# Kernel tuning notes

Measured on AMD Instinct MI355X. Metric: run time of the kernel, lower is better.

## Reference

```python
import jax, jax.numpy as jnp
import numpy as np

N, E, D_IN, H, C = 100000, 1600000, 256, 128, 10


def setup_inputs() -> dict:
    key = jax.random.key(0)
    ks = jax.random.split(key, 12)
    x = jax.random.normal(ks[0], (N, D_IN), dtype=jnp.float32)
    edge_index = jax.random.randint(ks[1], (2, E), 0, N, dtype=jnp.int64)
    reranker_scores = jax.random.normal(ks[2], (N,), dtype=jnp.float32)
    s_in = 1.0 / np.sqrt(D_IN)
    s_h = 1.0 / np.sqrt(H)
    # SAGEConv: lin_l applies to aggregated neighbors (with bias), lin_r to root (no bias)
    W_l = jax.random.uniform(ks[3], (H, D_IN), jnp.float32, -s_in, s_in)
    b_l = jax.random.uniform(ks[4], (H,), jnp.float32, -s_in, s_in)
    W_r = jax.random.uniform(ks[5], (H, D_IN), jnp.float32, -s_in, s_in)
    W_res = jax.random.uniform(ks[6], (H, D_IN), jnp.float32, -s_in, s_in)
    b_res = jax.random.uniform(ks[7], (H,), jnp.float32, -s_in, s_in)
    W_score = jax.random.uniform(ks[8], (1, H), jnp.float32, -s_h, s_h)
    b_score = jax.random.uniform(ks[9], (1,), jnp.float32, -s_h, s_h)
    W_crit = jax.random.uniform(ks[10], (C, H), jnp.float32, -s_h, s_h)
    b_crit = jax.random.uniform(ks[11], (C,), jnp.float32, -s_h, s_h)
    alpha = jnp.float32(0.65)
    return {"x": x, "edge_index": edge_index, "reranker_scores": reranker_scores,
            "W_l": W_l, "b_l": b_l, "W_r": W_r, "W_res": W_res, "b_res": b_res,
            "W_score": W_score, "b_score": b_score, "W_crit": W_crit, "b_crit": b_crit,
            "alpha": alpha}


def reference(x, edge_index, reranker_scores, W_l, b_l, W_r, W_res, b_res,
              W_score, b_score, W_crit, b_crit, alpha):
    src, dst = edge_index[0], edge_index[1]
    n = x.shape[0]
    ones = jnp.ones(src.shape[0], dtype=x.dtype)
    deg = jax.ops.segment_sum(ones, dst, num_segments=n)          # [N]
    nbr_sum = jax.ops.segment_sum(x[src], dst, num_segments=n)    # [N, D_IN]
    agg = nbr_sum / jnp.maximum(deg, 1.0)[:, None]                # mean aggregation
    # SAGEConv: lin_l(agg) + lin_r(x); relu; dropout (eval -> identity); residual
    h = jax.nn.relu(agg @ W_l.T + b_l + x @ W_r.T)                # [N, H]
    h = h + (x @ W_res.T + b_res)                                 # residual projection
    gnn_scores = (h @ W_score.T + b_score)[:, 0]                  # [N]
    a = jax.nn.sigmoid(alpha)
    final_scores = a * reranker_scores + (1.0 - a) * gnn_scores
    criterion_logits = h @ W_crit.T + b_crit                      # [N, C]
    return final_scores, criterion_logits
```

## Files before the change

kernel.cpp:

```cpp
#include <hip/hip_runtime.h>
#include <math.h>

#define DIN 256
#define HDIM 128
#define NCRIT 10
#define BSH 9
#define EPB 4096

typedef __bf16 bf16;
typedef bf16 bf16x8 __attribute__((ext_vector_type(8)));
typedef float f32x4 __attribute__((ext_vector_type(4)));
typedef float f32x2 __attribute__((ext_vector_type(2)));

static inline size_t alignup(size_t x, size_t a) { return (x + a - 1) & ~(a - 1); }

__device__ inline float bflo(unsigned v) { return __uint_as_float(v << 16); }
__device__ inline float bfhi(unsigned v) { return __uint_as_float(v & 0xffff0000u); }

__device__ inline bf16x8 cvt8(float4 v0, float4 v1) {
    bf16x8 w;
    w[0] = (bf16)v0.x; w[1] = (bf16)v0.y; w[2] = (bf16)v0.z; w[3] = (bf16)v0.w;
    w[4] = (bf16)v1.x; w[5] = (bf16)v1.y; w[6] = (bf16)v1.z; w[7] = (bf16)v1.w;
    return w;
}

__device__ inline void gl_lds16(const void* g, void* l) {
    __builtin_amdgcn_global_load_lds(
        (const __attribute__((address_space(1))) unsigned*)g,
        (__attribute__((address_space(3))) unsigned*)l, 16, 0, 0);
}

__global__ __launch_bounds__(256) void k_bucket2(
    const int* __restrict__ src, const int* __restrict__ dst, int E,
    int* __restrict__ bcnt, int2* __restrict__ bpool, int capb, int nB,
    const float* __restrict__ Wl, const float* __restrict__ Wr,
    const float* __restrict__ Wres,
    const float* __restrict__ wscore, const float* __restrict__ wcrit,
    bf16* __restrict__ WcatT)
{
    int t = threadIdx.x;
    int b = blockIdx.x;
    if (b < 64) {
        int base = (b * 256 + t) * 4;
        int r = base >> 8;
        int c0 = base & 255;
        const float* W = (r < 128) ? Wl : Wr;
        float4 v = *(const float4*)&W[(size_t)(r & 127) * 256 + c0];
        bf16 o[4] = {(bf16)v.x, (bf16)v.y, (bf16)v.z, (bf16)v.w};
        char* d = (char*)WcatT + ((((size_t)(c0 >> 3) * 272 + r) << 4) + ((c0 & 7) << 1));
        *(uint2*)d = *(const uint2*)o;
        return;
    } else if (b < 80) {
        int q = b - 64;
        int k = t;
        float s = 0.f;
        if (q < 11) {
            const float* wepi = (q == 0) ? wscore : &wcrit[(size_t)(q - 1) * HDIM];
            for (int c = 0; c < HDIM; ++c)
                s += wepi[c] * Wres[(size_t)c * 256 + k];
        }
        char* d = (char*)WcatT + ((((size_t)(k >> 3) * 272 + 256 + q) << 4) + ((k & 7) << 1));
        *(bf16*)d = (bf16)s;
        return;
    }

    __shared__ int lcnt[256], lbase[256], lcur[256], gbase[256];
    __shared__ int2 stage[EPB];

    int blk = b - 80;
    int base = blk * EPB;
    int m = min(EPB, E - base);
    if (m <= 0) return;

    lcnt[t] = 0;
    __syncthreads();
    for (int i = t; i < m; i += 256)
        atomicAdd(&lcnt[dst[base + i] >> BSH], 1);
    __syncthreads();
    int c0 = lcnt[t];
    for (int d = 1; d < 256; d <<= 1) {
        int a0 = lcnt[t];
        int b0 = (t >= d) ? lcnt[t - d] : 0;
        __syncthreads();
        lcnt[t] = a0 + b0;
        __syncthreads();
    }
    int e0 = lcnt[t] - c0;
    lbase[t] = e0;
    lcur[t] = e0;
    if (t < nB && c0 > 0) gbase[t] = atomicAdd(&bcnt[t * 16], c0);
    __syncthreads();
    for (int i = t; i < m; i += 256) {
        int s2 = src[base + i], d = dst[base + i];
        int bk = d >> BSH;
        int pos = atomicAdd(&lcur[bk], 1);
        stage[pos] = make_int2(s2, d);
    }
    __syncthreads();
    int wv = t >> 6, lane = t & 63;
    for (int bk = wv; bk < nB; bk += 4) {
        int lb = lbase[bk];
        int cb = lcnt[bk] - lb;
        if (cb == 0) continue;
        int gb = gbase[bk];
        int2* dstp = bpool + (size_t)bk * capb + gb;
        for (int j = lane; j < cb && gb + j < capb; j += 64)
            dstp[j] = stage[lb + j];
    }
}

__global__ __launch_bounds__(256) void k_fin(const int* __restrict__ bcnt,
                                             const int2* __restrict__ bpool, int capb,
                                             int n, int* __restrict__ off,
                                             int* __restrict__ cnt, int* __restrict__ sidx) {
    __shared__ int lcnt[512], lcur[512];
    int b = blockIdx.x, t = threadIdx.x;
    int m = min(bcnt[b * 16], capb);
    const int2* ep = bpool + (size_t)b * capb;

    lcnt[t] = 0; lcnt[t + 256] = 0;
    __syncthreads();
    for (int i = t; i < m; i += 256) {
        int2 e = ep[i];
        atomicAdd(&lcnt[e.y & 511], 1);
    }
    __syncthreads();
    int c0 = lcnt[t], c1 = lcnt[t + 256];
    for (int d = 1; d < 512; d <<= 1) {
        int a0 = lcnt[t], a1 = lcnt[t + 256];
        int b0 = (t >= d) ? lcnt[t - d] : 0;
        int b1 = ((t + 256) >= d) ? lcnt[t + 256 - d] : 0;
        __syncthreads();
        lcnt[t] = a0 + b0; lcnt[t + 256] = a1 + b1;
        __syncthreads();
    }
    int e0 = lcnt[t] - c0, e1 = lcnt[t + 256] - c1;
    int nbase = b << BSH;
    int sbase = b * capb;
    lcur[t] = e0; lcur[t + 256] = e1;
    int n0 = nbase + t, n1 = nbase + t + 256;
    if (n0 < n) { off[n0] = sbase + e0; cnt[n0] = c0; }
    if (n1 < n) { off[n1] = sbase + e1; cnt[n1] = c1; }
    __syncthreads();
    for (int i = t; i < m; i += 256) {
        int2 e = ep[i];
        int pos = atomicAdd(&lcur[e.y & 511], 1);
        sidx[sbase + pos] = e.x;
    }
}

__global__ __launch_bounds__(512) void k_gemm(
    const float* __restrict__ x, const bf16* __restrict__ WcatT, int n,
    unsigned char* __restrict__ yq, bf16* __restrict__ z, float* __restrict__ w)
{
    __shared__ __align__(16) char smem[147456];
    int t = threadIdx.x;
    int wv = t >> 6, lane = t & 63;
    int l15 = lane & 15, kq = lane >> 4;

    {
        int cbase0 = wv * 64;
        #pragma unroll
        for (int i = 0; i < 17; i++) {
            int cbase = i * 512 + cbase0;
            gl_lds16((const char*)WcatT + (((size_t)cbase + lane) << 4),
                     smem + ((size_t)cbase << 4));
        }
    }
    __syncthreads();

    char* scr = smem + 139264 + wv * 1024;
    int rrow = lane >> 2, rc4 = (lane & 3) * 4;

    int nTiles = (n + 127) >> 7;
    for (int tile = blockIdx.x; tile < nTiles; tile += gridDim.x) {
        int rowb = tile * 128 + wv * 16;
        int myrow = rowb + l15;
        const float* ap = x + (size_t)(myrow < n ? myrow : (n - 1)) * 256 + kq * 8;

        float4 xa[8], xb[8];
        #pragma unroll
        for (int s = 0; s < 8; s++) {
            xa[s] = *(const float4*)(ap + s * 32);
            xb[s] = *(const float4*)(ap + s * 32 + 4);
        }

        f32x4 acc[17];
        #pragma unroll
        for (int C = 0; C < 17; C++) acc[C] = (f32x4){0.f, 0.f, 0.f, 0.f};

        #pragma unroll
        for (int s = 0; s < 8; s++) {
            bf16x8 afr = cvt8(xa[s], xb[s]);
            int sbase = ((s * 4 + kq) * 272 + l15) << 4;
            #pragma unroll
            for (int C = 0; C < 17; C++) {
                bf16x8 b = *(const bf16x8*)(smem + sbase + C * 256);
                acc[C] = __builtin_amdgcn_mfma_f32_16x16x32_bf16(afr, b, acc[C], 0, 0, 0);
            }
        }

        int gr = rowb + rrow;
        bool ok = gr < n;
        #pragma unroll
        for (int C = 0; C < 17; C++) {
            #pragma unroll
            for (int j = 0; j < 4; j++)
                *(float*)(scr + ((((kq << 2) + j) * 16 + l15) << 2)) = acc[C][j];
            f32x4 vv = *(const f32x4*)(scr + ((rrow * 16 + rc4) << 2));
            if (C < 8) {
                unsigned pk = (unsigned)__builtin_amdgcn_cvt_pk_fp8_f32(vv[0], vv[1], 0, false);
                pk = (unsigned)__builtin_amdgcn_cvt_pk_fp8_f32(vv[2], vv[3], pk, true);
                if (ok) *(unsigned*)(yq + (size_t)gr * 128 + C * 16 + rc4) = pk;
            } else if (C < 16) {
                bf16 o[4] = {(bf16)vv[0], (bf16)vv[1], (bf16)vv[2], (bf16)vv[3]};
                if (ok) *(uint2*)((char*)z + (size_t)gr * 256 + (C - 8) * 32 + rc4 * 2) =
                            *(const uint2*)o;
            } else {
                if (ok) *(f32x4*)(w + (size_t)gr * 16 + rc4) = vv;
            }
        }
    }
}

__global__ __launch_bounds__(256) void k_gather(
    const unsigned char* __restrict__ yq, const bf16* __restrict__ z,
    const float* __restrict__ w,
    const int* __restrict__ off, const int* __restrict__ cnt, const int* __restrict__ sidx,
    const float* __restrict__ bl, const float* __restrict__ bres,
    const float* __restrict__ wscore, const float* __restrict__ bscore,
    const float* __restrict__ wcrit, const float* __restrict__ bcrit,
    const float* __restrict__ rrs, const float* __restrict__ palpha,
    int n, float* __restrict__ outF, float* __restrict__ outL)
{
    __shared__ bf16 wsb[11 * 128];
    int t = threadIdx.x;
    for (int i = t; i < 11 * 128; i += 256) {
        int q = i >> 7, c = i & 127;
        wsb[i] = (bf16)((q == 0) ? wscore[c] : wcrit[(size_t)(q - 1) * HDIM + c]);
    }
    __syncthreads();

    int node = blockIdx.x * 4 + (t >> 6);
    if (node >= n) return;
    int lane = t & 63, r2 = lane >> 5, c32 = lane & 31;

    uint2 zr = *(const uint2*)&z[(size_t)node * HDIM + c32 * 4];
    float wpre = (lane < 16) ? w[(size_t)node * 16 + lane] : 0.f;
    float4 blv = *(const float4*)&bl[c32 * 4];
    float4 brv = *(const float4*)&bres[c32 * 4];

    const unsigned char* ybase = yq + c32 * 4;
    int beg = off[node], len = cnt[node];
    const int* sp = sidx + beg;

    f32x2 a01 = {0.f, 0.f}, a23 = {0.f, 0.f};
    int e = 0;
    for (; e + 8 <= len; e += 8) {
        int i0 = sp[e + r2];
        int i1 = sp[e + 2 + r2];
        int i2 = sp[e + 4 + r2];
        int i3 = sp[e + 6 + r2];
        int v0 = *(const int*)(ybase + ((size_t)(unsigned)i0 << 7));
        int v1 = *(const int*)(ybase + ((size_t)(unsigned)i1 << 7));
        int v2 = *(const int*)(ybase + ((size_t)(unsigned)i2 << 7));
        int v3 = *(const int*)(ybase + ((size_t)(unsigned)i3 << 7));
        a01 += __builtin_amdgcn_cvt_pk_f32_fp8(v0, false)
             + __builtin_amdgcn_cvt_pk_f32_fp8(v1, false)
             + __builtin_amdgcn_cvt_pk_f32_fp8(v2, false)
             + __builtin_amdgcn_cvt_pk_f32_fp8(v3, false);
        a23 += __builtin_amdgcn_cvt_pk_f32_fp8(v0, true)
             + __builtin_amdgcn_cvt_pk_f32_fp8(v1, true)
             + __builtin_amdgcn_cvt_pk_f32_fp8(v2, true)
             + __builtin_amdgcn_cvt_pk_f32_fp8(v3, true);
    }
    for (; e < len; e += 2) {
        int slot = e + r2;
        int ii = sp[slot < len ? slot : len - 1];
        int v = *(const int*)(ybase + ((size_t)(unsigned)ii << 7));
        if (slot < len) {
            a01 += __builtin_amdgcn_cvt_pk_f32_fp8(v, false);
            a23 += __builtin_amdgcn_cvt_pk_f32_fp8(v, true);
        }
    }
    float a0 = a01[0], a1 = a01[1], a2 = a23[0], a3 = a23[1];
    a0 += __shfl_xor(a0, 32, 64);
    a1 += __shfl_xor(a1, 32, 64);
    a2 += __shfl_xor(a2, 32, 64);
    a3 += __shfl_xor(a3, 32, 64);
    float inv = 1.f / fmaxf((float)len, 1.f);

    float h0 = fmaxf(a0 * inv + blv.x + bflo(zr.x), 0.f) + brv.x;
    float h1 = fmaxf(a1 * inv + blv.y + bfhi(zr.x), 0.f) + brv.y;
    float h2 = fmaxf(a2 * inv + blv.z + bflo(zr.y), 0.f) + brv.z;
    float h3 = fmaxf(a3 * inv + blv.w + bfhi(zr.y), 0.f) + brv.w;

    float p[6], wq[6];
    #pragma unroll
    for (int qq = 0; qq < 6; qq++) {
        int q = r2 * 6 + qq;
        float s = 0.f;
        if (q < 11) {
            uint2 ww = *(const uint2*)&wsb[q * 128 + c32 * 4];
            s = h0 * bflo(ww.x) + h1 * bfhi(ww.x) + h2 * bflo(ww.y) + h3 * bfhi(ww.y);
        }
        #pragma unroll
        for (int d = 1; d < 32; d <<= 1)
            s += __shfl_xor(s, d, 64);
        p[qq] = s;
        wq[qq] = __shfl(wpre, (q < 11) ? q : 0, 64);
    }
    if ((lane & 31) == 0) {
        if (r2 == 0) {
            float al = palpha[0];
            float aa = 1.f / (1.f + expf(-al));
            outF[node] = aa * rrs[node] + (1.f - aa) * (p[0] + wq[0] + bscore[0]);
            #pragma unroll
            for (int qq = 1; qq < 6; qq++)
                outL[(size_t)node * NCRIT + qq - 1] = p[qq] + wq[qq] + bcrit[qq - 1];
        } else {
            #pragma unroll
            for (int qq = 0; qq < 5; qq++)
                outL[(size_t)node * NCRIT + 5 + qq] = p[qq] + wq[qq] + bcrit[5 + qq];
        }
    }
}

extern "C" void kernel_launch(void* const* d_in, const int* in_sizes, int n_in,
                              void* d_out, int out_size, void* d_ws, size_t ws_size,
                              hipStream_t stream) {
    const float* x      = (const float*)d_in[0];
    const int*   ei     = (const int*)d_in[1];
    const float* rrs    = (const float*)d_in[2];
    const float* Wl     = (const float*)d_in[3];
    const float* bl     = (const float*)d_in[4];
    const float* Wr     = (const float*)d_in[5];
    const float* Wres   = (const float*)d_in[6];
    const float* bres   = (const float*)d_in[7];
    const float* wscore = (const float*)d_in[8];
    const float* bscore = (const float*)d_in[9];
    const float* wcrit  = (const float*)d_in[10];
    const float* bcrit  = (const float*)d_in[11];
    const float* alpha  = (const float*)d_in[12];

    int N = in_sizes[0] / DIN;
    int E = in_sizes[1] / 2;
    const int* srcv = ei;
    const int* dstv = ei + E;

    int nB = (N + 511) >> BSH;
    int capb = (E / (nB > 0 ? nB : 1)) * 2 + 256;

    char* p = (char*)d_ws;
    int* bcnt  = (int*)p; p += alignup((size_t)nB * 16 * 4, 256);
    int2* bpool = (int2*)p; p += alignup((size_t)nB * capb * 8, 256);
    int* off   = (int*)p; p += alignup((size_t)N * 4, 256);
    int* cnt   = (int*)p; p += alignup((size_t)N * 4, 256);
    int* sidx  = (int*)p; p += alignup((size_t)nB * capb * 4, 256);
    bf16* WcatT = (bf16*)p; p += alignup((size_t)32 * 272 * 16, 256);
    unsigned char* yq = (unsigned char*)p; p += alignup((size_t)N * HDIM, 256);
    bf16* z    = (bf16*)p; p += alignup((size_t)N * HDIM * 2, 256);
    float* w   = (float*)p; p += alignup((size_t)N * 16 * 4, 256);

    hipMemsetAsync(bcnt, 0, (size_t)nB * 16 * 4, stream);

    k_bucket2<<<80 + (E + EPB - 1) / EPB, 256, 0, stream>>>(
        srcv, dstv, E, bcnt, bpool, capb, nB, Wl, Wr, Wres, wscore, wcrit, WcatT);
    k_fin<<<nB, 256, 0, stream>>>(bcnt, bpool, capb, N, off, cnt, sidx);

    k_gemm<<<256, 512, 0, stream>>>(x, WcatT, N, yq, z, w);

    float* outF = (float*)d_out;
    float* outL = outF + N;
    k_gather<<<(N + 3) / 4, 256, 0, stream>>>(yq, z, w, off, cnt, sidx, bl, bres,
                                              wscore, bscore, wcrit, bcrit,
                                              rrs, alpha, N, outF, outL);
}
```

Baseline: 185.6 us.

## Fold biases into GEMM and precomputed epilogue constants; widen gather loads to 8 bytes

The b_l bias is now added in the GEMM epilogue before the bf16 store of z. The b_res contributions to the score and criterion heads, plus their biases, are precomputed once into an 11-element constant buffer by an extra block in the bucket kernel. The gather kernel is restructured so each lane handles 8 features with 8-byte fp8 loads across 4 edge groups of 16 lanes, instead of 4 features with 4-byte loads across 2 groups. This reduces per-node bias loads, the number of shuffles in the reductions and the number of gather load instructions, at the cost of more registers per lane and a slightly different rounding point for b_l.

```diff
diff --git a/kernel.cpp b/kernel.cpp
--- a/kernel.cpp
+++ b/kernel.cpp
@@ -36,7 +36,9 @@
     const float* __restrict__ Wl, const float* __restrict__ Wr,
     const float* __restrict__ Wres,
     const float* __restrict__ wscore, const float* __restrict__ wcrit,
-    bf16* __restrict__ WcatT)
+    const float* __restrict__ bres, const float* __restrict__ bscore,
+    const float* __restrict__ bcrit,
+    bf16* __restrict__ WcatT, float* __restrict__ cq)
 {
     int t = threadIdx.x;
     int b = blockIdx.x;
@@ -62,12 +64,20 @@
         char* d = (char*)WcatT + ((((size_t)(k >> 3) * 272 + 256 + q) << 4) + ((k & 7) << 1));
         *(bf16*)d = (bf16)s;
         return;
+    } else if (b == 80) {
+        if (t < 11) {
+            const float* wepi = (t == 0) ? wscore : &wcrit[(size_t)(t - 1) * HDIM];
+            float s = 0.f;
+            for (int c = 0; c < HDIM; ++c) s += bres[c] * wepi[c];
+            cq[t] = s + ((t == 0) ? bscore[0] : bcrit[t - 1]);
+        }
+        return;
     }
 
     __shared__ int lcnt[256], lbase[256], lcur[256], gbase[256];
     __shared__ int2 stage[EPB];
 
-    int blk = b - 80;
+    int blk = b - 81;
     int base = blk * EPB;
     int m = min(EPB, E - base);
     if (m <= 0) return;
@@ -151,7 +161,8 @@
 
 __global__ __launch_bounds__(512) void k_gemm(
     const float* __restrict__ x, const bf16* __restrict__ WcatT, int n,
-    unsigned char* __restrict__ yq, bf16* __restrict__ z, float* __restrict__ w)
+    unsigned char* __restrict__ yq, bf16* __restrict__ z, float* __restrict__ w,
+    const float* __restrict__ bl)
 {
     __shared__ __align__(16) char smem[147456];
     int t = threadIdx.x;
@@ -213,7 +224,9 @@
                 pk = (unsigned)__builtin_amdgcn_cvt_pk_fp8_f32(vv[2], vv[3], pk, true);
                 if (ok) *(unsigned*)(yq + (size_t)gr * 128 + C * 16 + rc4) = pk;
             } else if (C < 16) {
-                bf16 o[4] = {(bf16)vv[0], (bf16)vv[1], (bf16)vv[2], (bf16)vv[3]};
+                float4 blv = *(const float4*)&bl[(C - 8) * 16 + rc4];
+                bf16 o[4] = {(bf16)(vv[0] + blv.x), (bf16)(vv[1] + blv.y),
+                             (bf16)(vv[2] + blv.z), (bf16)(vv[3] + blv.w)};
                 if (ok) *(uint2*)((char*)z + (size_t)gr * 256 + (C - 8) * 32 + rc4 * 2) =
                             *(const uint2*)o;
             } else {
@@ -225,11 +238,9 @@
 
 __global__ __launch_bounds__(256) void k_gather(
     const unsigned char* __restrict__ yq, const bf16* __restrict__ z,
-    const float* __restrict__ w,
+    const float* __restrict__ w, const float* __restrict__ cq,
     const int* __restrict__ off, const int* __restrict__ cnt, const int* __restrict__ sidx,
-    const float* __restrict__ bl, const float* __restrict__ bres,
-    const float* __restrict__ wscore, const float* __restrict__ bscore,
-    const float* __restrict__ wcrit, const float* __restrict__ bcrit,
+    const float* __restrict__ wscore, const float* __restrict__ wcrit,
     const float* __restrict__ rrs, const float* __restrict__ palpha,
     int n, float* __restrict__ outF, float* __restrict__ outL)
 {
@@ -243,85 +254,86 @@
 
     int node = blockIdx.x * 4 + (t >> 6);
     if (node >= n) return;
-    int lane = t & 63, r2 = lane >> 5, c32 = lane & 31;
-
-    uint2 zr = *(const uint2*)&z[(size_t)node * HDIM + c32 * 4];
-    float wpre = (lane < 16) ? w[(size_t)node * 16 + lane] : 0.f;
-    float4 blv = *(const float4*)&bl[c32 * 4];
-    float4 brv = *(const float4*)&bres[c32 * 4];
-
-    const unsigned char* ybase = yq + c32 * 4;
+    int lane = t & 63, g4 = lane >> 4, c16 = lane & 15;
+
+    uint4 zv = *(const uint4*)((const char*)z + (size_t)node * 256 + c16 * 16);
+
+    const unsigned char* ybase = yq + c16 * 8;
     int beg = off[node], len = cnt[node];
     const int* sp = sidx + beg;
 
-    f32x2 a01 = {0.f, 0.f}, a23 = {0.f, 0.f};
+    f32x2 a01 = {0.f, 0.f}, a23 = {0.f, 0.f}, a45 = {0.f, 0.f}, a67 = {0.f, 0.f};
     int e = 0;
     for (; e + 8 <= len; e += 8) {
-        int i0 = sp[e + r2];
-        int i1 = sp[e + 2 + r2];
-        int i2 = sp[e + 4 + r2];
-        int i3 = sp[e + 6 + r2];
-        int v0 = *(const int*)(ybase + ((size_t)(unsigned)i0 << 7));
-        int v1 = *(const int*)(ybase + ((size_t)(unsigned)i1 << 7));
-        int v2 = *(const int*)(ybase + ((size_t)(unsigned)i2 << 7));
-        int v3 = *(const int*)(ybase + ((size_t)(unsigned)i3 << 7));
-        a01 += __builtin_amdgcn_cvt_pk_f32_fp8(v0, false)
-             + __builtin_amdgcn_cvt_pk_f32_fp8(v1, false)
-             + __builtin_amdgcn_cvt_pk_f32_fp8(v2, false)
-             + __builtin_amdgcn_cvt_pk_f32_fp8(v3, false);
-        a23 += __builtin_amdgcn_cvt_pk_f32_fp8(v0, true)
-             + __builtin_amdgcn_cvt_pk_f32_fp8(v1, true)
-             + __builtin_amdgcn_cvt_pk_f32_fp8(v2, true)
-             + __builtin_amdgcn_cvt_pk_f32_fp8(v3, true);
-    }
-    for (; e < len; e += 2) {
-        int slot = e + r2;
+        int i0 = sp[e + g4];
+        int i1 = sp[e + 4 + g4];
+        uint2 v0 = *(const uint2*)(ybase + ((size_t)(unsigned)i0 << 7));
+        uint2 v1 = *(const uint2*)(ybase + ((size_t)(unsigned)i1 << 7));
+        a01 += __builtin_amdgcn_cvt_pk_f32_fp8(v0.x, false)
+             + __builtin_amdgcn_cvt_pk_f32_fp8(v1.x, false);
+        a23 += __builtin_amdgcn_cvt_pk_f32_fp8(v0.x, true)
+             + __builtin_amdgcn_cvt_pk_f32_fp8(v1.x, true);
+        a45 += __builtin_amdgcn_cvt_pk_f32_fp8(v0.y, false)
+             + __builtin_amdgcn_cvt_pk_f32_fp8(v1.y, false);
+        a67 += __builtin_amdgcn_cvt_pk_f32_fp8(v0.y, true)
+             + __builtin_amdgcn_cvt_pk_f32_fp8(v1.y, true);
+    }
+    for (; e < len; e += 4) {
+        int slot = e + g4;
         int ii = sp[slot < len ? slot : len - 1];
-        int v = *(const int*)(ybase + ((size_t)(unsigned)ii << 7));
+        uint2 v = *(const uint2*)(ybase + ((size_t)(unsigned)ii << 7));
         if (slot < len) {
-            a01 += __builtin_amdgcn_cvt_pk_f32_fp8(v, false);
-            a23 += __builtin_amdgcn_cvt_pk_f32_fp8(v, true);
-        }
-    }
-    float a0 = a01[0], a1 = a01[1], a2 = a23[0], a3 = a23[1];
-    a0 += __shfl_xor(a0, 32, 64);
-    a1 += __shfl_xor(a1, 32, 64);
-    a2 += __shfl_xor(a2, 32, 64);
-    a3 += __shfl_xor(a3, 32, 64);
+            a01 += __builtin_amdgcn_cvt_pk_f32_fp8(v.x, false);
+            a23 += __builtin_amdgcn_cvt_pk_f32_fp8(v.x, true);
+            a45 += __builtin_amdgcn_cvt_pk_f32_fp8(v.y, false);
+            a67 += __builtin_amdgcn_cvt_pk_f32_fp8(v.y, true);
+        }
+    }
+    float a[8] = {a01[0], a01[1], a23[0], a23[1], a45[0], a45[1], a67[0], a67[1]};
+    #pragma unroll
+    for (int j = 0; j < 8; j++) {
+        a[j] += __shfl_xor(a[j], 16, 64);
+        a[j] += __shfl_xor(a[j], 32, 64);
+    }
     float inv = 1.f / fmaxf((float)len, 1.f);
 
-    float h0 = fmaxf(a0 * inv + blv.x + bflo(zr.x), 0.f) + brv.x;
-    float h1 = fmaxf(a1 * inv + blv.y + bfhi(zr.x), 0.f) + brv.y;
-    float h2 = fmaxf(a2 * inv + blv.z + bflo(zr.y), 0.f) + brv.z;
-    float h3 = fmaxf(a3 * inv + blv.w + bfhi(zr.y), 0.f) + brv.w;
-
-    float p[6], wq[6];
+    float zf[8] = {bflo(zv.x), bfhi(zv.x), bflo(zv.y), bfhi(zv.y),
+                   bflo(zv.z), bfhi(zv.z), bflo(zv.w), bfhi(zv.w)};
+    float h[8];
     #pragma unroll
-    for (int qq = 0; qq < 6; qq++) {
-        int q = r2 * 6 + qq;
+    for (int j = 0; j < 8; j++)
+        h[j] = fmaxf(a[j] * inv + zf[j], 0.f);
+
+    float p[3];
+    #pragma unroll
+    for (int qq = 0; qq < 3; qq++) {
+        int q = g4 * 3 + qq;
         float s = 0.f;
         if (q < 11) {
-            uint2 ww = *(const uint2*)&wsb[q * 128 + c32 * 4];
-            s = h0 * bflo(ww.x) + h1 * bfhi(ww.x) + h2 * bflo(ww.y) + h3 * bfhi(ww.y);
-        }
-        #pragma unroll
-        for (int d = 1; d < 32; d <<= 1)
+            uint4 ww = *(const uint4*)&wsb[q * 128 + c16 * 8];
+            s = h[0] * bflo(ww.x) + h[1] * bfhi(ww.x)
+              + h[2] * bflo(ww.y) + h[3] * bfhi(ww.y)
+              + h[4] * bflo(ww.z) + h[5] * bfhi(ww.z)
+              + h[6] * bflo(ww.w) + h[7] * bfhi(ww.w);
+        }
+        #pragma unroll
+        for (int d = 1; d < 16; d <<= 1)
             s += __shfl_xor(s, d, 64);
         p[qq] = s;
-        wq[qq] = __shfl(wpre, (q < 11) ? q : 0, 64);
-    }
-    if ((lane & 31) == 0) {
-        if (r2 == 0) {
-            float al = palpha[0];
-            float aa = 1.f / (1.f + expf(-al));
-            outF[node] = aa * rrs[node] + (1.f - aa) * (p[0] + wq[0] + bscore[0]);
-            #pragma unroll
-            for (int qq = 1; qq < 6; qq++)
-                outL[(size_t)node * NCRIT + qq - 1] = p[qq] + wq[qq] + bcrit[qq - 1];
-        } else {
-            #pragma unroll
-            for (int qq = 0; qq < 5; qq++)
-                outL[(size_t)node * NCRIT + 5 + qq] = p[qq] + wq[qq] + bcrit[5 + qq];
+    }
+    if (c16 == 0) {
+        #pragma unroll
+        for (int qq = 0; qq < 3; qq++) {
+            int q = g4 * 3 + qq;
+            if (q >= 11) continue;
+            float val = p[qq] + w[(size_t)node * 16 + q] + cq[q];
+            if (q == 0) {
+                float al = palpha[0];
+                float aa = 1.f / (1.f + expf(-al));
+                outF[node] = aa * rrs[node] + (1.f - aa) * val;
+            } else {
+                outL[(size_t)node * NCRIT + q - 1] = val;
+            }
         }
     }
 }
@@ -361,18 +373,19 @@
     unsigned char* yq = (unsigned char*)p; p += alignup((size_t)N * HDIM, 256);
     bf16* z    = (bf16*)p; p += alignup((size_t)N * HDIM * 2, 256);
     float* w   = (float*)p; p += alignup((size_t)N * 16 * 4, 256);
+    float* cq  = (float*)p; p += 256;
 
     hipMemsetAsync(bcnt, 0, (size_t)nB * 16 * 4, stream);
 
-    k_bucket2<<<80 + (E + EPB - 1) / EPB, 256, 0, stream>>>(
-        srcv, dstv, E, bcnt, bpool, capb, nB, Wl, Wr, Wres, wscore, wcrit, WcatT);
+    k_bucket2<<<81 + (E + EPB - 1) / EPB, 256, 0, stream>>>(
+        srcv, dstv, E, bcnt, bpool, capb, nB, Wl, Wr, Wres, wscore, wcrit,
+        bres, bscore, bcrit, WcatT, cq);
     k_fin<<<nB, 256, 0, stream>>>(bcnt, bpool, capb, N, off, cnt, sidx);
 
-    k_gemm<<<256, 512, 0, stream>>>(x, WcatT, N, yq, z, w);
+    k_gemm<<<256, 512, 0, stream>>>(x, WcatT, N, yq, z, w, bl);
 
     float* outF = (float*)d_out;
     float* outL = outF + N;
-    k_gather<<<(N + 3) / 4, 256, 0, stream>>>(yq, z, w, off, cnt, sidx, bl, bres,
-                                              wscore, bscore, wcrit, bcrit,
-                                              rrs, alpha, N, outF, outL);
-}
+    k_gather<<<(N + 3) / 4, 256, 0, stream>>>(yq, z, w, cq, off, cnt, sidx,
+                                              wscore, wcrit, rrs, alpha, N, outF, outL);
+}
```

After: 185.6 us. Within noise of the previous version (-0.0%).
